# Kernel optimization log

Hardware: AMD Instinct MI355X
Metric: run time of the kernel (lower is better)

The kernel has to match this reference:

```python
import jax, jax.numpy as jnp
import numpy as np

N_NODES = 100000
N_EDGES = 3200000
F_IN = 512
F_OUT = 512
T_ITERS = 4
EPS = 1e-5


def setup_inputs() -> dict:
    key = jax.random.key(0)
    k1, k2, k3, k4, k5 = jax.random.split(key, 5)
    x = jax.random.normal(k1, (N_NODES, F_IN), dtype=jnp.float32)
    stdv = 1.0 / np.sqrt(F_OUT)
    weight = jax.random.uniform(k2, (F_IN, F_OUT), dtype=jnp.float32,
                                minval=-stdv, maxval=stdv)
    adj_rows = jax.random.randint(k3, (N_EDGES,), 0, N_NODES, dtype=jnp.int32)
    adj_cols = jax.random.randint(k4, (N_EDGES,), 0, N_NODES, dtype=jnp.int32)
    adj_vals = jax.random.uniform(k5, (N_EDGES,), dtype=jnp.float32)
    return {"x": x, "weight": weight, "adj_rows": adj_rows,
            "adj_cols": adj_cols, "adj_vals": adj_vals}


def oni_norm(weight):
    # norm_groups=1: Z is [in_features, out_features]
    Zc = weight - weight.mean(axis=-1, keepdims=True)
    S = Zc @ Zc.T + EPS * jnp.eye(Zc.shape[0], dtype=weight.dtype)
    norm_S = jnp.linalg.norm(S)  # Frobenius norm (scalar)
    S = S / norm_S
    B = jnp.eye(S.shape[-1], dtype=weight.dtype)
    for _ in range(T_ITERS):
        # baddbmm(1.5, B, -0.5, B^3, S) = 1.5*B - 0.5*(B@B@B)@S
        B3 = B @ B @ B
        B = 1.5 * B - 0.5 * (B3 @ S)
    W = (B @ Zc) / jnp.sqrt(norm_S)
    return W


def reference(x, weight, adj_rows, adj_cols, adj_vals):
    # Faithful to the torch forward: ONINorm(W) is computed (self.W) but the
    # dense mm uses the raw self.weight, exactly as in the source.
    W = oni_norm(weight)  # noqa: F841 (computed but unused, as in original)
    support = x @ weight                       # [N, F_OUT]
    # spmm: out[r] = sum_e adj_vals[e] * support[cols[e]] for rows[e] == r
    gathered = adj_vals[:, None] * support[adj_cols]  # [E, F_OUT]
    output = jax.ops.segment_sum(gathered, adj_rows, num_segments=N_NODES)
    return output
```

## Files before the change

### kernel.cpp

```cpp
#include <hip/hip_runtime.h>
#include <hip/hip_bf16.h>

#define N_NODESC 100000
#define N_EDGESC 3200000
#define FDIM 512
#define MPAD 100096
#define NBLK 256
#define EPB 12500
#define NBUCKB 391
#define NCNT (NBLK * NBUCKB)
#define NB_SCAN ((NCNT + 8191) / 8192)

typedef __attribute__((ext_vector_type(4))) float f32x4;
typedef __attribute__((ext_vector_type(8))) __bf16 bf16x8;
typedef unsigned long long u64;

__device__ __forceinline__ void gload_lds16(const void* g, void* l) {
  __builtin_amdgcn_global_load_lds(
      (const __attribute__((address_space(1))) unsigned int*)g,
      (__attribute__((address_space(3))) unsigned int*)l, 16, 0, 0);
}

__global__ __launch_bounds__(256) void k_bcount_wt(const int* __restrict__ rows,
                                                   int* __restrict__ cnt,
                                                   const float* __restrict__ w,
                                                   __bf16* __restrict__ wT) {
  __shared__ int h[NBUCKB];
  if (blockIdx.x >= NBLK) {
    const int b = blockIdx.x - NBLK;
    const int i0 = b * 1024 + threadIdx.x * 4;
    #pragma unroll
    for (int q = 0; q < 4; ++q) {
      const int j = i0 + q;
      const int k = j >> 9, n = j & (FDIM - 1);
      wT[n * FDIM + k] = (__bf16)w[j];
    }
    return;
  }
  const int blk = blockIdx.x;
  for (int i = threadIdx.x; i < NBUCKB; i += 256) h[i] = 0;
  __syncthreads();
  const int e0 = blk * EPB;
  for (int e = e0 + threadIdx.x; e < e0 + EPB; e += 256)
    atomicAdd(&h[rows[e] >> 8], 1);
  __syncthreads();
  for (int i = threadIdx.x; i < NBUCKB; i += 256) cnt[i * NBLK + blk] = h[i];
}

__global__ __launch_bounds__(1024) void k_scan1(int* __restrict__ d, int* __restrict__ bsum) {
  __shared__ int s[1024];
  const int t = threadIdx.x;
  const int base = blockIdx.x * 8192 + t * 8;
  int v[8];
  int sum = 0;
  #pragma unroll
  for (int k = 0; k < 8; ++k) {
    v[k] = (base + k < NCNT) ? d[base + k] : 0;
    sum += v[k];
  }
  s[t] = sum;
  __syncthreads();
  for (int dl = 1; dl < 1024; dl <<= 1) {
    int a = s[t];
    int b = (t >= dl) ? s[t - dl] : 0;
    __syncthreads();
    s[t] = a + b;
    __syncthreads();
  }
  int excl = (t == 0) ? 0 : s[t - 1];
  #pragma unroll
  for (int k = 0; k < 8; ++k) {
    if (base + k < NCNT) d[base + k] = excl;
    excl += v[k];
  }
  if (t == 1023) bsum[blockIdx.x] = s[1023];
}

__global__ __launch_bounds__(64) void k_scan2(int* __restrict__ bsum) {
  const int t = threadIdx.x;
  int v = (t < NB_SCAN) ? bsum[t] : 0;
  #pragma unroll
  for (int dl = 1; dl < 64; dl <<= 1) {
    const int u = __shfl_up(v, dl, 64);
    if (t >= dl) v += u;
  }
  if (t < NB_SCAN) {
    const int excl = v - bsum[t];
    bsum[t] = excl;
  }
}

__global__ __launch_bounds__(512) void k_bscatter(const int* __restrict__ rows,
                                                  const int* __restrict__ cols,
                                                  const float* __restrict__ vals,
                                                  const int* __restrict__ off,
                                                  const int* __restrict__ bsum,
                                                  u64* __restrict__ bedges) {
  __shared__ int lofs[NBUCKB];
  __shared__ int lcur[NBUCKB];
  const int blk = blockIdx.x;
  for (int i = threadIdx.x; i < NBUCKB; i += 512) {
    const int idx = i * NBLK + blk;
    lofs[i] = off[idx] + bsum[idx >> 13];
    lcur[i] = 0;
  }
  __syncthreads();
  const int e0 = blk * EPB;
  for (int e = e0 + threadIdx.x; e < e0 + EPB; e += 512) {
    const int r = rows[e];
    const int b = r >> 8;
    const int p = lofs[b] + atomicAdd(&lcur[b], 1);
    bedges[p] = ((u64)__float_as_uint(vals[e]) << 32) |
                ((u64)(r & 255) << 17) | (unsigned)cols[e];
  }
}

__global__ __launch_bounds__(512) void k_csr(const int* __restrict__ off,
                                             const int* __restrict__ bsum,
                                             const u64* __restrict__ bedges,
                                             u64* __restrict__ edges,
                                             int* __restrict__ row_off) {
  __shared__ int hcnt[256];
  __shared__ int hcur[256];
  const int b = blockIdx.x;
  const int t = threadIdx.x;
  const int i0 = b * NBLK;
  const int i1 = (b + 1) * NBLK;
  const int base  = off[i0] + bsum[i0 >> 13];
  const int nextb = (b + 1 < NBUCKB) ? (off[i1] + bsum[i1 >> 13]) : N_EDGESC;
  if (t < 256) hcnt[t] = 0;
  __syncthreads();
  for (int j = base + t; j < nextb; j += 512)
    atomicAdd(&hcnt[(int)(bedges[j] >> 17) & 255], 1);
  __syncthreads();
  for (int d = 1; d < 256; d <<= 1) {
    int a = 0;
    if (t < 256) a = hcnt[t];
    int u = (t >= d && t < 256) ? hcnt[t - d] : 0;
    __syncthreads();
    if (t < 256) hcnt[t] = a + u;
    __syncthreads();
  }
  if (t < 256) {
    const int excl = (t == 0) ? 0 : hcnt[t - 1];
    row_off[b * 256 + t] = base + excl;
    hcur[t] = base + excl;
  }
  __syncthreads();
  for (int j = base + t; j < nextb; j += 512) {
    const u64 e = bedges[j];
    const int lr = (int)(e >> 17) & 255;
    const int p = atomicAdd(&hcur[lr], 1);
    edges[p] = (e & 0xFFFFFFFF0001FFFFull) & ~0x1FFE0000ull;
  }
}

__global__ __launch_bounds__(512) void k_gemm(const float* __restrict__ x,
                                              const __bf16* __restrict__ wT,
                                              __bf16* __restrict__ support) {
  __shared__ __bf16 lA[2][128 * 32];
  __shared__ __bf16 lB[2][512 * 32];
  const int tm = blockIdx.x;
  const int tid = threadIdx.x;
  const int wid = tid >> 6;
  const int lane = tid & 63;
  const int wm = wid >> 2;
  const int wn = wid & 3;

  const long rowA0 = (long)tm * 128;

  const int srow  = lane >> 2;
  const int skoff = (lane & 3) * 8;

  const int arow = tid >> 2;
  const int ah   = (tid & 3) * 8;

  f32x4 acc[4][8];
  #pragma unroll
  for (int m = 0; m < 4; ++m)
    #pragma unroll
    for (int n = 0; n < 8; ++n)
      acc[m][n] = (f32x4){0.f, 0.f, 0.f, 0.f};

  const long grow = rowA0 + arow;
  const long arowc = (grow < N_NODESC) ? grow : (N_NODESC - 1);
  const bool apad = grow >= N_NODESC;

  float4 ar[2];
  auto issueA = [&](int kt) {
    const int k0 = kt * 32;
    ar[0] = *(const float4*)(x + arowc * FDIM + k0 + ah);
    ar[1] = *(const float4*)(x + arowc * FDIM + k0 + ah + 4);
  };
  auto writeA = [&](int buf) {
    bf16x8 o;
    o[0] = (__bf16)(apad ? 0.f : ar[0].x);
    o[1] = (__bf16)(apad ? 0.f : ar[0].y);
    o[2] = (__bf16)(apad ? 0.f : ar[0].z);
    o[3] = (__bf16)(apad ? 0.f : ar[0].w);
    o[4] = (__bf16)(apad ? 0.f : ar[1].x);
    o[5] = (__bf16)(apad ? 0.f : ar[1].y);
    o[6] = (__bf16)(apad ? 0.f : ar[1].z);
    o[7] = (__bf16)(apad ? 0.f : ar[1].w);
    *(bf16x8*)&lA[buf][arow * 32 + ah] = o;
  };
  auto stageB = [&](int buf, int kt) {
    const int k0 = kt * 32;
    #pragma unroll
    for (int it = 0; it < 4; ++it) {
      const int c = wid * 4 + it;
      const __bf16* gB = wT + (long)(c * 16 + srow) * FDIM + k0 + skoff;
      gload_lds16(gB, &lB[buf][c * 512]);
    }
  };

  issueA(0);
  stageB(0, 0);
  writeA(0);
  __syncthreads();

  const int frow = lane & 15;
  const int fk   = (lane >> 4) * 8;

  for (int kt = 0; kt < 16; ++kt) {
    const int buf = kt & 1;
    if (kt < 15) {
      issueA(kt + 1);
      stageB(buf ^ 1, kt + 1);
    }
    bf16x8 a[4], b[8];
    #pragma unroll
    for (int m = 0; m < 4; ++m)
      a[m] = *(const bf16x8*)&lA[buf][(wm * 64 + m * 16 + frow) * 32 + fk];
    #pragma unroll
    for (int n = 0; n < 8; ++n)
      b[n] = *(const bf16x8*)&lB[buf][(wn * 128 + n * 16 + frow) * 32 + fk];
    #pragma unroll
    for (int m = 0; m < 4; ++m)
      #pragma unroll
      for (int n = 0; n < 8; ++n)
        acc[m][n] = __builtin_amdgcn_mfma_f32_16x16x32_bf16(a[m], b[n], acc[m][n], 0, 0, 0);
    if (kt < 15) writeA(buf ^ 1);
    __syncthreads();
  }

  const long crow0 = (long)tm * 128 + wm * 64 + (lane >> 4) * 4;
  const int  ccol0 = wn * 128 + frow;
  #pragma unroll
  for (int m = 0; m < 4; ++m)
    #pragma unroll
    for (int n = 0; n < 8; ++n)
      #pragma unroll
      for (int i = 0; i < 4; ++i)
        support[(crow0 + m * 16 + i) * (long)FDIM + ccol0 + n * 16] = (__bf16)acc[m][n][i];
}

__global__ __launch_bounds__(256) void k_spmm(const int* __restrict__ row_off,
                                              const u64* __restrict__ edges,
                                              const __bf16* __restrict__ support,
                                              float* __restrict__ out) {
  const int r = blockIdx.x * 4 + (threadIdx.x >> 6);
  const int lane = threadIdx.x & 63;
  if (r >= N_NODESC) return;
  const int beg = row_off[r];
  const int end = (r + 1 < N_NODESC) ? row_off[r + 1] : N_EDGESC;
  const __bf16* sp = support + lane * 8;

  float acc[8];
  #pragma unroll
  for (int i = 0; i < 8; ++i) acc[i] = 0.f;

  int j = beg;
  for (; j + 1 < end; j += 2) {
    const u64 e0 = edges[j];
    const u64 e1 = edges[j + 1];
    const bf16x8 s0 = *(const bf16x8*)(sp + (long)(unsigned)(e0 & 0xffffffffu) * FDIM);
    const bf16x8 s1 = *(const bf16x8*)(sp + (long)(unsigned)(e1 & 0xffffffffu) * FDIM);
    const float v0 = __uint_as_float((unsigned)(e0 >> 32));
    const float v1 = __uint_as_float((unsigned)(e1 >> 32));
    #pragma unroll
    for (int i = 0; i < 8; ++i) acc[i] += v0 * (float)s0[i];
    #pragma unroll
    for (int i = 0; i < 8; ++i) acc[i] += v1 * (float)s1[i];
  }
  if (j < end) {
    const u64 e0 = edges[j];
    const bf16x8 s0 = *(const bf16x8*)(sp + (long)(unsigned)(e0 & 0xffffffffu) * FDIM);
    const float v0 = __uint_as_float((unsigned)(e0 >> 32));
    #pragma unroll
    for (int i = 0; i < 8; ++i) acc[i] += v0 * (float)s0[i];
  }

  *(float4*)(out + (long)r * FDIM + lane * 8) =
      make_float4(acc[0], acc[1], acc[2], acc[3]);
  *(float4*)(out + (long)r * FDIM + lane * 8 + 4) =
      make_float4(acc[4], acc[5], acc[6], acc[7]);
}

extern "C" void kernel_launch(void* const* d_in, const int* in_sizes, int n_in,
                              void* d_out, int out_size, void* d_ws, size_t ws_size,
                              hipStream_t stream) {
  const float* x    = (const float*)d_in[0];
  const float* w    = (const float*)d_in[1];
  const int*   rows = (const int*)d_in[2];
  const int*   cols = (const int*)d_in[3];
  const float* vals = (const float*)d_in[4];
  float* out = (float*)d_out;

  char* ws = (char*)d_ws;
  size_t off = 0;
  auto alloc = [&](size_t bytes) {
    void* p = ws + off;
    off += (bytes + 255) & ~(size_t)255;
    return p;
  };
  __bf16* support = (__bf16*)alloc((size_t)MPAD * FDIM * 2);
  __bf16* wT      = (__bf16*)alloc((size_t)FDIM * FDIM * 2);
  int*    cnt     = (int*)alloc((size_t)(NCNT + 1) * 4);
  int*    row_off = (int*)alloc((size_t)(MPAD + 1) * 4);
  int*    bsum    = (int*)alloc(1024 * 4);
  u64*    edges   = (u64*)alloc((size_t)N_EDGESC * 8);
  u64*    bedges  = (u64*)alloc((size_t)N_EDGESC * 8);
  (void)ws_size;

  k_bcount_wt<<<NBLK + 256, 256, 0, stream>>>(rows, cnt, w, wT);
  k_scan1<<<NB_SCAN, 1024, 0, stream>>>(cnt, bsum);
  k_scan2<<<1, 64, 0, stream>>>(bsum);
  k_bscatter<<<NBLK, 512, 0, stream>>>(rows, cols, vals, cnt, bsum, bedges);
  k_csr<<<NBUCKB, 512, 0, stream>>>(cnt, bsum, bedges, edges, row_off);
  k_gemm<<<MPAD / 128, 512, 0, stream>>>(x, wT, support);
  k_spmm<<<N_NODESC / 4, 256, 0, stream>>>(row_off, edges, support, out);
}
```

Measured before the change: 698.4 us.

## Fold block-sum scan into consumers and read GEMM B operand directly from global

Removes the separate single-wave k_scan2 launch by having k_bscatter and k_csr each compute the exclusive prefix of the few scan block sums in shared memory. This drops one kernel launch and its dependency bubble at the cost of a little redundant work per block. In the GEMM, the B (weight) tile is no longer staged through LDS with async global-to-LDS loads; each wave loads its bf16 fragments straight from global/L2. This frees LDS and removes the B staging, but adds uncached-latency global loads inside the MFMA loop with no double buffering. The edge mask expression is also rewritten equivalently.

```diff
diff --git a/kernel.cpp b/kernel.cpp
--- a/kernel.cpp
+++ b/kernel.cpp
@@ -76,17 +76,17 @@
   if (t == 1023) bsum[blockIdx.x] = s[1023];
 }
 
-__global__ __launch_bounds__(64) void k_scan2(int* __restrict__ bsum) {
-  const int t = threadIdx.x;
-  int v = (t < NB_SCAN) ? bsum[t] : 0;
-  #pragma unroll
-  for (int dl = 1; dl < 64; dl <<= 1) {
-    const int u = __shfl_up(v, dl, 64);
-    if (t >= dl) v += u;
-  }
-  if (t < NB_SCAN) {
-    const int excl = v - bsum[t];
-    bsum[t] = excl;
+__device__ __forceinline__ void prefix_bsum(const int* __restrict__ bsum, int* E) {
+  if (threadIdx.x < 64) {
+    const int t = threadIdx.x;
+    int raw = (t < NB_SCAN) ? bsum[t] : 0;
+    int v = raw;
+    #pragma unroll
+    for (int dl = 1; dl < 16; dl <<= 1) {
+      const int u = __shfl_up(v, dl, 64);
+      if (t >= dl) v += u;
+    }
+    if (t < NB_SCAN) E[t] = v - raw;
   }
 }
 
@@ -96,12 +96,15 @@
                                                   const int* __restrict__ off,
                                                   const int* __restrict__ bsum,
                                                   u64* __restrict__ bedges) {
+  __shared__ int E[16];
   __shared__ int lofs[NBUCKB];
   __shared__ int lcur[NBUCKB];
   const int blk = blockIdx.x;
+  prefix_bsum(bsum, E);
+  __syncthreads();
   for (int i = threadIdx.x; i < NBUCKB; i += 512) {
     const int idx = i * NBLK + blk;
-    lofs[i] = off[idx] + bsum[idx >> 13];
+    lofs[i] = off[idx] + E[idx >> 13];
     lcur[i] = 0;
   }
   __syncthreads();
@@ -120,16 +123,18 @@
                                              const u64* __restrict__ bedges,
                                              u64* __restrict__ edges,
                                              int* __restrict__ row_off) {
+  __shared__ int E[16];
   __shared__ int hcnt[256];
   __shared__ int hcur[256];
   const int b = blockIdx.x;
   const int t = threadIdx.x;
+  prefix_bsum(bsum, E);
+  if (t < 256) hcnt[t] = 0;
+  __syncthreads();
   const int i0 = b * NBLK;
   const int i1 = (b + 1) * NBLK;
-  const int base  = off[i0] + bsum[i0 >> 13];
-  const int nextb = (b + 1 < NBUCKB) ? (off[i1] + bsum[i1 >> 13]) : N_EDGESC;
-  if (t < 256) hcnt[t] = 0;
-  __syncthreads();
+  const int base  = off[i0] + E[i0 >> 13];
+  const int nextb = (b + 1 < NBUCKB) ? (off[i1] + E[i1 >> 13]) : N_EDGESC;
   for (int j = base + t; j < nextb; j += 512)
     atomicAdd(&hcnt[(int)(bedges[j] >> 17) & 255], 1);
   __syncthreads();
@@ -151,7 +156,7 @@
     const u64 e = bedges[j];
     const int lr = (int)(e >> 17) & 255;
     const int p = atomicAdd(&hcur[lr], 1);
-    edges[p] = (e & 0xFFFFFFFF0001FFFFull) & ~0x1FFE0000ull;
+    edges[p] = (e & 0xFFFFFFFF00000000ull) | (e & 0x1FFFFull);
   }
 }
 
@@ -159,7 +164,6 @@
                                               const __bf16* __restrict__ wT,
                                               __bf16* __restrict__ support) {
   __shared__ __bf16 lA[2][128 * 32];
-  __shared__ __bf16 lB[2][512 * 32];
   const int tm = blockIdx.x;
   const int tid = threadIdx.x;
   const int wid = tid >> 6;
@@ -168,9 +172,6 @@
   const int wn = wid & 3;
 
   const long rowA0 = (long)tm * 128;
-
-  const int srow  = lane >> 2;
-  const int skoff = (lane & 3) * 8;
 
   const int arow = tid >> 2;
   const int ah   = (tid & 3) * 8;
@@ -204,37 +205,25 @@
     o[7] = (__bf16)(apad ? 0.f : ar[1].w);
     *(bf16x8*)&lA[buf][arow * 32 + ah] = o;
   };
-  auto stageB = [&](int buf, int kt) {
-    const int k0 = kt * 32;
-    #pragma unroll
-    for (int it = 0; it < 4; ++it) {
-      const int c = wid * 4 + it;
-      const __bf16* gB = wT + (long)(c * 16 + srow) * FDIM + k0 + skoff;
-      gload_lds16(gB, &lB[buf][c * 512]);
-    }
-  };
 
   issueA(0);
-  stageB(0, 0);
   writeA(0);
   __syncthreads();
 
   const int frow = lane & 15;
   const int fk   = (lane >> 4) * 8;
+  const __bf16* wbase = wT + (long)(wn * 128 + frow) * FDIM + fk;
 
   for (int kt = 0; kt < 16; ++kt) {
     const int buf = kt & 1;
-    if (kt < 15) {
-      issueA(kt + 1);
-      stageB(buf ^ 1, kt + 1);
-    }
+    if (kt < 15) issueA(kt + 1);
     bf16x8 a[4], b[8];
     #pragma unroll
     for (int m = 0; m < 4; ++m)
       a[m] = *(const bf16x8*)&lA[buf][(wm * 64 + m * 16 + frow) * 32 + fk];
     #pragma unroll
     for (int n = 0; n < 8; ++n)
-      b[n] = *(const bf16x8*)&lB[buf][(wn * 128 + n * 16 + frow) * 32 + fk];
+      b[n] = *(const bf16x8*)(wbase + (long)n * 16 * FDIM + kt * 32);
     #pragma unroll
     for (int m = 0; m < 4; ++m)
       #pragma unroll
@@ -325,7 +314,6 @@
 
   k_bcount_wt<<<NBLK + 256, 256, 0, stream>>>(rows, cnt, w, wT);
   k_scan1<<<NB_SCAN, 1024, 0, stream>>>(cnt, bsum);
-  k_scan2<<<1, 64, 0, stream>>>(bsum);
   k_bscatter<<<NBLK, 512, 0, stream>>>(rows, cols, vals, cnt, bsum, bedges);
   k_csr<<<NBUCKB, 512, 0, stream>>>(cnt, bsum, bedges, edges, row_off);
   k_gemm<<<MPAD / 128, 512, 0, stream>>>(x, wT, support);
```

After: 749.8 us. +7.4%, slower.
